# Performance work log

Measured on AMD Instinct MI355X. Metric: run time of the kernel, lower is better.

## Reference

```python
import jax, jax.numpy as jnp
import numpy as np

D = 384      # d_model
DM = 256     # memory feature dim
DF = 1536    # dim_feedforward
EPS = 1e-5


def _layer_norm(x, g, b):
    m = jnp.mean(x, axis=-1, keepdims=True)
    v = jnp.mean(jnp.square(x - m), axis=-1, keepdims=True)
    return (x - m) * jax.lax.rsqrt(v + EPS) * g + b


def setup_inputs() -> dict:
    key = jax.random.key(0)
    ks = jax.random.split(key, 24)
    B, T, T1, Tc = 8, 2048, 2048, 2048
    s = 0.02
    inp = {
        "tgt": jax.random.normal(ks[0], (B, T, D), jnp.float32),
        "memory": jax.random.normal(ks[1], (B, T1, DM), jnp.float32),
        "a1": jnp.float32(0.5),
        "score_c": jax.random.normal(ks[2], (B, 1, Tc, T1), jnp.float32) * 0.1,
        "out_c": jax.random.normal(ks[3], (B, Tc, D), jnp.float32),
        # attention projections
        "Wq": jax.random.normal(ks[4], (D, D), jnp.float32) * s,
        "bq": jnp.zeros((D,), jnp.float32),
        "Wk": jax.random.normal(ks[5], (DM, D), jnp.float32) * s,
        "bk": jnp.zeros((D,), jnp.float32),
        "Wv": jax.random.normal(ks[6], (DM, D), jnp.float32) * s,
        "bv": jnp.zeros((D,), jnp.float32),
        "Wu": jax.random.normal(ks[7], (D, D), jnp.float32) * s,  # unknown
        "bu": jnp.zeros((D,), jnp.float32),
        "Wn": jax.random.normal(ks[8], (D, D), jnp.float32) * s,  # known
        "bn": jnp.zeros((D,), jnp.float32),
        # FFN
        "W1": jax.random.normal(ks[9], (D, DF), jnp.float32) * s,
        "b1": jnp.zeros((DF,), jnp.float32),
        "W2": jax.random.normal(ks[10], (DF, D), jnp.float32) * s,
        "b2": jnp.zeros((D,), jnp.float32),
        # LayerNorms
        "g1": jnp.ones((D,), jnp.float32),
        "be1": jnp.zeros((D,), jnp.float32),
        "g2": jnp.ones((D,), jnp.float32),
        "be2": jnp.zeros((D,), jnp.float32),
    }
    return inp


def reference(tgt, memory, a1, score_c, out_c,
              Wq, bq, Wk, bk, Wv, bv, Wu, bu, Wn, bn,
              W1, b1, W2, b2, g1, be1, g2, be2):
    # --- En_De_Attention (n_head = 1; dropout p=0 / eval mode -> identity) ---
    scale = 1.0 / jnp.sqrt(jnp.float32(D))
    q = tgt @ Wq + bq                  # [B,T,D]
    k = memory @ Wk + bk               # [B,T1,D]
    v = memory @ Wv + bv               # [B,T1,D]
    att = jnp.einsum('btd,bsd->bts', q, k) * scale            # [B,T,T1]

    unknow = tgt @ Wu + bu             # [B,T,D]
    know = out_c @ Wn + bn             # [B,Tc,D]
    score1 = jnp.einsum('btd,bcd->btc', unknow, know) * scale  # [B,T,Tc]
    mixed = jnp.einsum('btc,bcs->bts', score1, score_c[:, 0])  # [B,T,T1]

    # tt = a1 in (0,1]: blended-score branch of the original module
    score = a1 * jax.nn.softmax(mixed, axis=-1) \
          + (1.0 - a1) * jax.nn.softmax(att, axis=-1)          # [B,T,T1]
    z = jnp.einsum('bts,bsd->btd', score, v)                   # [B,T,D]

    # --- residual + norm1 ---
    x = _layer_norm(tgt + z, g1, be1)
    # --- FFN (relu) + residual + norm2 (dropout eval -> identity) ---
    ff = jax.nn.relu(x @ W1 + b1) @ W2 + b2
    out = _layer_norm(x + ff, g2, be2)
    # score2 returned with head dim, matching torch shape [B,1,T,T1]
    return out, score[:, None]
```

## Files before the change

kernel.cpp:

```cpp
#include <hip/hip_runtime.h>
#include <stdint.h>

typedef __attribute__((ext_vector_type(8))) short bf16x8;
typedef __attribute__((ext_vector_type(4))) float f32x4;

__device__ __forceinline__ short f2bf(float f) {
    union { float f; unsigned u; } v; v.f = f;
    unsigned r = v.u + 0x7fffu + ((v.u >> 16) & 1u);
    return (short)(r >> 16);
}
__device__ __forceinline__ float bf2f(short s) {
    union { unsigned u; float f; } v;
    v.u = ((unsigned)(unsigned short)s) << 16;
    return v.f;
}

__device__ __forceinline__ void gld16(const void* g, void* l) {
    auto gp = reinterpret_cast<const __attribute__((address_space(1))) unsigned int*>(
        reinterpret_cast<uintptr_t>(g));
    auto lp = reinterpret_cast<__attribute__((address_space(3))) unsigned int*>(
        reinterpret_cast<uintptr_t>(l));
    __builtin_amdgcn_global_load_lds(gp, lp, 16, 0, 0);
}

template<int OUTBF, int BIASMODE , int DORELU>
__global__ __launch_bounds__(256, 2) void gemm128p(
    const short* __restrict__ Ag, const short* __restrict__ Bg,
    void* __restrict__ Cg, const float* __restrict__ bias,
    int K, int lda, int ldb, int ldc,
    long long sA, long long sB, long long sC, float scale)
{
    __shared__ short lds[2 * 16384];
    const int t = threadIdx.x;
    const int lane = t & 63;
    const int wave = t >> 6;
    const int wm = wave >> 1, wn = wave & 1;

    const int gx = gridDim.x, gy = gridDim.y;
    const int nwg = gx * gy * gridDim.z;
    int id = blockIdx.x + gx * (blockIdx.y + gy * blockIdx.z);
    id = (id & 7) * (nwg >> 3) + (id >> 3);
    const int bx = id % gx;
    const int by = (id / gx) % gy;
    const int bz = id / (gx * gy);

    const long long row0 = (long long)by * 128;
    const long long col0 = (long long)bx * 128;
    const int NT = K >> 6;

    const int srow = t >> 3;
    const int gk = ((t & 7) ^ (srow & 7)) * 8;
    const short* Asrc = Ag + (long long)bz * sA + (row0 + srow) * (long long)lda + gk;
    const short* Bsrc = Bg + (long long)bz * sB + (col0 + srow) * (long long)ldb + gk;

    const int frow = lane & 15;
    const int fq = lane >> 4;

    f32x4 acc[4][4] = {};

#define STAGE_A(WB, KC) do { _Pragma("unroll") \
        for (int r = 0; r < 4; ++r) \
            gld16(Asrc + (KC) + (long long)r * 32 * lda, &lds[(WB) + t * 8 + r * 2048]); } while (0)
#define STAGE_B(WB, KC) do { _Pragma("unroll") \
        for (int r = 0; r < 4; ++r) \
            gld16(Bsrc + (KC) + (long long)r * 32 * ldb, &lds[(WB) + 8192 + t * 8 + r * 2048]); } while (0)
#define RD_A(RB, M, KS) (*(const bf16x8*)&lds[(RB) + (wm * 64 + (M) * 16 + frow) * 64 + \
        ((((KS) << 2) | fq) ^ (frow & 7)) * 8])
#define RD_B(RB, Nn, KS) (*(const bf16x8*)&lds[(RB) + 8192 + (wn * 64 + (Nn) * 16 + frow) * 64 + \
        ((((KS) << 2) | fq) ^ (frow & 7)) * 8])

    STAGE_A(0, 0);
    STAGE_B(0, 0);
    asm volatile("s_waitcnt vmcnt(0)\ns_barrier" ::: "memory");

    for (int kt = 0; kt < NT; ++kt) {
        const int rb = (kt & 1) << 14;
        const int wb = ((kt + 1) & 1) << 14;
        const bool st = (kt + 1) < NT;
        const long long kc = (long long)(kt + 1) << 6;

        bf16x8 av[4], bv[4];

#pragma unroll
        for (int m = 0; m < 4; ++m) av[m] = RD_A(rb, m, 0);
#pragma unroll
        for (int n = 0; n < 4; ++n) bv[n] = RD_B(rb, n, 0);
        if (st) STAGE_A(wb, kc);
        asm volatile("s_barrier" ::: "memory");
        __builtin_amdgcn_s_setprio(1);
#pragma unroll
        for (int m = 0; m < 4; ++m)
#pragma unroll
            for (int n = 0; n < 4; ++n)
                acc[m][n] = __builtin_amdgcn_mfma_f32_16x16x32_bf16(av[m], bv[n], acc[m][n], 0, 0, 0);
        __builtin_amdgcn_s_setprio(0);
        asm volatile("s_barrier" ::: "memory");

#pragma unroll
        for (int m = 0; m < 4; ++m) av[m] = RD_A(rb, m, 1);
#pragma unroll
        for (int n = 0; n < 4; ++n) bv[n] = RD_B(rb, n, 1);
        if (st) STAGE_B(wb, kc);
        asm volatile("s_barrier" ::: "memory");
        __builtin_amdgcn_s_setprio(1);
#pragma unroll
        for (int m = 0; m < 4; ++m)
#pragma unroll
            for (int n = 0; n < 4; ++n)
                acc[m][n] = __builtin_amdgcn_mfma_f32_16x16x32_bf16(av[m], bv[n], acc[m][n], 0, 0, 0);
        __builtin_amdgcn_s_setprio(0);
        if (st) asm volatile("s_waitcnt vmcnt(0)\ns_barrier" ::: "memory");
        else    asm volatile("s_barrier" ::: "memory");
    }
#undef STAGE_A
#undef STAGE_B

    const int crow = (lane >> 4) * 4;
    const int ccol = lane & 15;
    const long long cz = (long long)bz * sC;
#pragma unroll
    for (int m = 0; m < 4; ++m)
#pragma unroll
        for (int n = 0; n < 4; ++n)
#pragma unroll
            for (int i = 0; i < 4; ++i) {
                long long r = row0 + wm * 64 + m * 16 + crow + i;
                long long c = col0 + wn * 64 + n * 16 + ccol;
                float v = acc[m][n][i] * scale;
                if (BIASMODE == 1) v += bias[c];
                if (BIASMODE == 2) v += bias[r];
                if (DORELU) v = fmaxf(v, 0.0f);
                long long idx = cz + r * (long long)ldc + c;
                if (OUTBF) ((short*)Cg)[idx] = f2bf(v);
                else ((float*)Cg)[idx] = v;
            }
}

__global__ __launch_bounds__(256, 2) void gemm128pz(
    const short* __restrict__ A1, const short* __restrict__ B1, short* __restrict__ C1,
    const float* __restrict__ bias1, int K1, int lda1, int ldb1, int ldc1,
    long long sB1, long long sC1,
    const short* __restrict__ A2, const short* __restrict__ B2, short* __restrict__ C2,
    const float* __restrict__ bias2, int K2, int lda2, int ldb2, int ldc2,
    long long sB2, long long sC2)
{
    __shared__ short lds[2 * 16384];
    const int t = threadIdx.x;
    const int lane = t & 63;
    const int wave = t >> 6;
    const int wm = wave >> 1, wn = wave & 1;

    const int gx = gridDim.x, gy = gridDim.y;
    const int nwg = gx * gy * gridDim.z;
    int id = blockIdx.x + gx * (blockIdx.y + gy * blockIdx.z);
    id = (id & 7) * (nwg >> 3) + (id >> 3);
    const int bx = id % gx;
    const int by = (id / gx) % gy;
    const int bz = id / (gx * gy);

    const bool sel = bz >= 8;
    const int zz = bz & 7;
    const short* Ag = sel ? A2 : A1;
    const short* Bg = sel ? B2 : B1;
    short* Cg = sel ? C2 : C1;
    const float* bias = sel ? bias2 : bias1;
    const int K = sel ? K2 : K1;
    const int lda = sel ? lda2 : lda1;
    const int ldb = sel ? ldb2 : ldb1;
    const int ldc = sel ? ldc2 : ldc1;
    const long long sB = sel ? sB2 : sB1;
    const long long sC = sel ? sC2 : sC1;

    const long long row0 = (long long)by * 128;
    const long long col0 = (long long)bx * 128;
    const int NT = K >> 6;

    const int srow = t >> 3;
    const int gk = ((t & 7) ^ (srow & 7)) * 8;
    const short* Asrc = Ag + (row0 + srow) * (long long)lda + gk;
    const short* Bsrc = Bg + (long long)zz * sB + (col0 + srow) * (long long)ldb + gk;

    const int frow = lane & 15;
    const int fq = lane >> 4;

    f32x4 acc[4][4] = {};

#define STAGE_A(WB, KC) do { _Pragma("unroll") \
        for (int r = 0; r < 4; ++r) \
            gld16(Asrc + (KC) + (long long)r * 32 * lda, &lds[(WB) + t * 8 + r * 2048]); } while (0)
#define STAGE_B(WB, KC) do { _Pragma("unroll") \
        for (int r = 0; r < 4; ++r) \
            gld16(Bsrc + (KC) + (long long)r * 32 * ldb, &lds[(WB) + 8192 + t * 8 + r * 2048]); } while (0)

    STAGE_A(0, 0);
    STAGE_B(0, 0);
    asm volatile("s_waitcnt vmcnt(0)\ns_barrier" ::: "memory");

    for (int kt = 0; kt < NT; ++kt) {
        const int rb = (kt & 1) << 14;
        const int wb = ((kt + 1) & 1) << 14;
        const bool st = (kt + 1) < NT;
        const long long kc = (long long)(kt + 1) << 6;

        bf16x8 av[4], bv[4];

#pragma unroll
        for (int m = 0; m < 4; ++m) av[m] = RD_A(rb, m, 0);
#pragma unroll
        for (int n = 0; n < 4; ++n) bv[n] = RD_B(rb, n, 0);
        if (st) STAGE_A(wb, kc);
        asm volatile("s_barrier" ::: "memory");
        __builtin_amdgcn_s_setprio(1);
#pragma unroll
        for (int m = 0; m < 4; ++m)
#pragma unroll
            for (int n = 0; n < 4; ++n)
                acc[m][n] = __builtin_amdgcn_mfma_f32_16x16x32_bf16(av[m], bv[n], acc[m][n], 0, 0, 0);
        __builtin_amdgcn_s_setprio(0);
        asm volatile("s_barrier" ::: "memory");

#pragma unroll
        for (int m = 0; m < 4; ++m) av[m] = RD_A(rb, m, 1);
#pragma unroll
        for (int n = 0; n < 4; ++n) bv[n] = RD_B(rb, n, 1);
        if (st) STAGE_B(wb, kc);
        asm volatile("s_barrier" ::: "memory");
        __builtin_amdgcn_s_setprio(1);
#pragma unroll
        for (int m = 0; m < 4; ++m)
#pragma unroll
            for (int n = 0; n < 4; ++n)
                acc[m][n] = __builtin_amdgcn_mfma_f32_16x16x32_bf16(av[m], bv[n], acc[m][n], 0, 0, 0);
        __builtin_amdgcn_s_setprio(0);
        if (st) asm volatile("s_waitcnt vmcnt(0)\ns_barrier" ::: "memory");
        else    asm volatile("s_barrier" ::: "memory");
    }
#undef STAGE_A
#undef STAGE_B

    const int crow = (lane >> 4) * 4;
    const int ccol = lane & 15;
    const long long cz = (long long)zz * sC;
#pragma unroll
    for (int m = 0; m < 4; ++m)
#pragma unroll
        for (int n = 0; n < 4; ++n)
#pragma unroll
            for (int i = 0; i < 4; ++i) {
                long long r = row0 + wm * 64 + m * 16 + crow + i;
                long long c = col0 + wn * 64 + n * 16 + ccol;
                float v = acc[m][n][i] + bias[r];
                Cg[cz + r * (long long)ldc + c] = f2bf(v);
            }
}

__global__ __launch_bounds__(256, 2) void gemm128dd(
    const short* __restrict__ Ag, const short* __restrict__ Bg, short* __restrict__ Cg,
    int K, int lda, int ldb, int ldc,
    long long sA, long long sB, long long sC,
    int dA, long long dB, long long dC, float scale)
{
    __shared__ short lds[2 * 16384];
    const int t = threadIdx.x;
    const int lane = t & 63;
    const int wave = t >> 6;
    const int wm = wave >> 1, wn = wave & 1;

    const int gx = gridDim.x, gy = gridDim.y;
    const int nwg = gx * gy * gridDim.z;
    int id = blockIdx.x + gx * (blockIdx.y + gy * blockIdx.z);
    id = (id & 7) * (nwg >> 3) + (id >> 3);
    const int bx = id % gx;
    const int by = (id / gx) % gy;
    const int bz = id / (gx * gy);

    const long long row0 = (long long)by * 128;
    const long long col0 = (long long)bx * 128;
    const int NT = K >> 6;

    const int srow = t >> 3;
    const int gk = ((t & 7) ^ (srow & 7)) * 8;
    const short* Asrc = Ag + (long long)bz * sA + (row0 + srow) * (long long)lda + gk;
    const short* Bsrc = Bg + (long long)bz * sB + (col0 + srow) * (long long)ldb + gk;

    const int frow = lane & 15;
    const int fq = lane >> 4;

    f32x4 accA[4][4] = {};
    f32x4 accB[4][4] = {};

#define AOFF(KT2) (((KT2) >= NT) ? ((long long)dA + (long long)((KT2) - NT) * 64) : ((long long)(KT2) * 64))
#define BOFF(KT2) (((KT2) >= NT) ? (dB + (long long)((KT2) - NT) * 64) : ((long long)(KT2) * 64))
#define STAGE_A(WB, OFF) do { _Pragma("unroll") \
        for (int r = 0; r < 4; ++r) \
            gld16(Asrc + (OFF) + (long long)r * 32 * lda, &lds[(WB) + t * 8 + r * 2048]); } while (0)
#define STAGE_B(WB, OFF) do { _Pragma("unroll") \
        for (int r = 0; r < 4; ++r) \
            gld16(Bsrc + (OFF) + (long long)r * 32 * ldb, &lds[(WB) + 8192 + t * 8 + r * 2048]); } while (0)

    STAGE_A(0, 0);
    STAGE_B(0, 0);
    asm volatile("s_waitcnt vmcnt(0)\ns_barrier" ::: "memory");

    const int NT2 = NT * 2;
    for (int kt = 0; kt < NT2; ++kt) {
        const int rb = (kt & 1) << 14;
        const int wb = ((kt + 1) & 1) << 14;
        const bool st = (kt + 1) < NT2;
        const long long ao = AOFF(kt + 1);
        const long long bo = BOFF(kt + 1);
        const bool first = kt < NT;

        bf16x8 av[4], bv[4];

#pragma unroll
        for (int m = 0; m < 4; ++m) av[m] = RD_A(rb, m, 0);
#pragma unroll
        for (int n = 0; n < 4; ++n) bv[n] = RD_B(rb, n, 0);
        if (st) STAGE_A(wb, ao);
        asm volatile("s_barrier" ::: "memory");
        __builtin_amdgcn_s_setprio(1);
        if (first) {
#pragma unroll
            for (int m = 0; m < 4; ++m)
#pragma unroll
                for (int n = 0; n < 4; ++n)
                    accA[m][n] = __builtin_amdgcn_mfma_f32_16x16x32_bf16(av[m], bv[n], accA[m][n], 0, 0, 0);
        } else {
#pragma unroll
            for (int m = 0; m < 4; ++m)
#pragma unroll
                for (int n = 0; n < 4; ++n)
                    accB[m][n] = __builtin_amdgcn_mfma_f32_16x16x32_bf16(av[m], bv[n], accB[m][n], 0, 0, 0);
        }
        __builtin_amdgcn_s_setprio(0);
        asm volatile("s_barrier" ::: "memory");

#pragma unroll
        for (int m = 0; m < 4; ++m) av[m] = RD_A(rb, m, 1);
#pragma unroll
        for (int n = 0; n < 4; ++n) bv[n] = RD_B(rb, n, 1);
        if (st) STAGE_B(wb, bo);
        asm volatile("s_barrier" ::: "memory");
        __builtin_amdgcn_s_setprio(1);
        if (first) {
#pragma unroll
            for (int m = 0; m < 4; ++m)
#pragma unroll
                for (int n = 0; n < 4; ++n)
                    accA[m][n] = __builtin_amdgcn_mfma_f32_16x16x32_bf16(av[m], bv[n], accA[m][n], 0, 0, 0);
        } else {
#pragma unroll
            for (int m = 0; m < 4; ++m)
#pragma unroll
                for (int n = 0; n < 4; ++n)
                    accB[m][n] = __builtin_amdgcn_mfma_f32_16x16x32_bf16(av[m], bv[n], accB[m][n], 0, 0, 0);
        }
        __builtin_amdgcn_s_setprio(0);
        if (st) asm volatile("s_waitcnt vmcnt(0)\ns_barrier" ::: "memory");
        else    asm volatile("s_barrier" ::: "memory");
    }
#undef STAGE_A
#undef STAGE_B
#undef AOFF
#undef BOFF
#undef RD_A
#undef RD_B

    const int crow = (lane >> 4) * 4;
    const int ccol = lane & 15;
    const long long cz = (long long)bz * sC;
#pragma unroll
    for (int m = 0; m < 4; ++m)
#pragma unroll
        for (int n = 0; n < 4; ++n)
#pragma unroll
            for (int i = 0; i < 4; ++i) {
                long long r = row0 + wm * 64 + m * 16 + crow + i;
                long long c = col0 + wn * 64 + n * 16 + ccol;
                long long idx = cz + r * (long long)ldc + c;
                Cg[idx] = f2bf(accA[m][n][i] * scale);
                Cg[idx + dC] = f2bf(accB[m][n][i] * scale);
            }
}

__global__ __launch_bounds__(256) void cast_all(
    const float* __restrict__ tgt, const float* __restrict__ mem, const float* __restrict__ outc,
    const float* __restrict__ bq, const float* __restrict__ bu,
    short* __restrict__ tgtb, short* __restrict__ memb, short* __restrict__ outcb,
    float* __restrict__ qubias)
{
    const long long R1 = 1572864;
    const long long R2 = R1 + 1048576;
    const long long R3 = R2 + 1572864;
    const long long R4 = R3 + 192;
    long long i = (long long)blockIdx.x * 256 + threadIdx.x;
    const float* in; short* out; long long j;
    if (i < R1) { in = tgt; out = tgtb; j = i; }
    else if (i < R2) { in = mem; out = memb; j = i - R1; }
    else if (i < R3) { in = outc; out = outcb; j = i - R2; }
    else if (i < R4) {
        j = i - R3;
        ((float4*)qubias)[j] = (j < 96) ? ((const float4*)bq)[j] : ((const float4*)bu)[j - 96];
        return;
    } else return;
    float4 v = ((const float4*)in)[j];
    short4 o;
    o.x = f2bf(v.x); o.y = f2bf(v.y); o.z = f2bf(v.z); o.w = f2bf(v.w);
    ((short4*)out)[j] = o;
}

__global__ __launch_bounds__(256) void transpose_all(
    const float* __restrict__ Wq, const float* __restrict__ Wk, const float* __restrict__ Wv,
    const float* __restrict__ Wu, const float* __restrict__ Wn,
    const float* __restrict__ W1, const float* __restrict__ W2,
    short* __restrict__ WquT, short* __restrict__ WkT, short* __restrict__ WvT,
    short* __restrict__ WnT, short* __restrict__ W1T, short* __restrict__ W2T)
{
    __shared__ float tile[64][65];
    int b = blockIdx.x;
    const float* in; short* out; int R, C, local;
    if (b < 36)       { in = Wq; out = WquT;          R = 384;  C = 384;  local = b; }
    else if (b < 60)  { in = Wk; out = WkT;           R = 256;  C = 384;  local = b - 36; }
    else if (b < 84)  { in = Wv; out = WvT;           R = 256;  C = 384;  local = b - 60; }
    else if (b < 120) { in = Wu; out = WquT + 147456; R = 384;  C = 384;  local = b - 84; }
    else if (b < 156) { in = Wn; out = WnT;           R = 384;  C = 384;  local = b - 120; }
    else if (b < 300) { in = W1; out = W1T;           R = 384;  C = 1536; local = b - 156; }
    else              { in = W2; out = W2T;           R = 1536; C = 384;  local = b - 300; }
    const int nbx = C >> 6;
    const int r0 = (local / nbx) * 64, c0 = (local % nbx) * 64;
    const int lr = threadIdx.x >> 6, lc = threadIdx.x & 63;
#pragma unroll
    for (int i = 0; i < 16; ++i) {
        int r = lr * 16 + i;
        tile[r][lc] = in[(long long)(r0 + r) * C + c0 + lc];
    }
    __syncthreads();
#pragma unroll
    for (int i = 0; i < 16; ++i) {
        int r = lr * 16 + i;
        out[(long long)(c0 + r) * R + r0 + lc] = f2bf(tile[lc][r]);
    }
}

__global__ __launch_bounds__(256) void transpose_cast(
    const float* __restrict__ in, short* __restrict__ out,
    int R, int C, long long sIn, long long sOut)
{
    __shared__ float tile[64][65];
    const long long zi = (long long)blockIdx.z * sIn;
    const long long zo = (long long)blockIdx.z * sOut;
    const int r0 = blockIdx.y * 64, c0 = blockIdx.x * 64;
    const int lr = threadIdx.x >> 6, lc = threadIdx.x & 63;
#pragma unroll
    for (int i = 0; i < 16; ++i) {
        int r = lr * 16 + i;
        tile[r][lc] = in[zi + (long long)(r0 + r) * C + c0 + lc];
    }
    __syncthreads();
#pragma unroll
    for (int i = 0; i < 16; ++i) {
        int r = lr * 16 + i;
        out[zo + (long long)(c0 + r) * R + r0 + lc] = f2bf(tile[lc][r]);
    }
}

__global__ __launch_bounds__(256) void softmax_blend(
    const short* __restrict__ attb, const short* __restrict__ mixb,
    const float* __restrict__ a1p,
    float* __restrict__ outF, short* __restrict__ outB)
{
    const int S = 2048;
    const long long row = blockIdx.x;
    const short* ar = attb + row * S;
    const short* mr = mixb + row * S;
    const int t = threadIdx.x;
    const int wave = t >> 6;

    bf16x8 a8 = *(const bf16x8*)&ar[t * 8];
    bf16x8 m8 = *(const bf16x8*)&mr[t * 8];
    float av[8], mv[8];
#pragma unroll
    for (int i = 0; i < 8; ++i) { av[i] = bf2f(a8[i]); mv[i] = bf2f(m8[i]); }

    float amax = av[0], mmax = mv[0];
#pragma unroll
    for (int i = 1; i < 8; ++i) { amax = fmaxf(amax, av[i]); mmax = fmaxf(mmax, mv[i]); }
#pragma unroll
    for (int o = 32; o; o >>= 1) {
        amax = fmaxf(amax, __shfl_xor(amax, o));
        mmax = fmaxf(mmax, __shfl_xor(mmax, o));
    }
    __shared__ float red[2][4];
    if ((t & 63) == 0) { red[0][wave] = amax; red[1][wave] = mmax; }
    __syncthreads();
    amax = fmaxf(fmaxf(red[0][0], red[0][1]), fmaxf(red[0][2], red[0][3]));
    mmax = fmaxf(fmaxf(red[1][0], red[1][1]), fmaxf(red[1][2], red[1][3]));

    float asum = 0.f, msum = 0.f;
#pragma unroll
    for (int i = 0; i < 8; ++i) {
        av[i] = __expf(av[i] - amax); asum += av[i];
        mv[i] = __expf(mv[i] - mmax); msum += mv[i];
    }
#pragma unroll
    for (int o = 32; o; o >>= 1) {
        asum += __shfl_xor(asum, o);
        msum += __shfl_xor(msum, o);
    }
    __shared__ float red2[2][4];
    if ((t & 63) == 0) { red2[0][wave] = asum; red2[1][wave] = msum; }
    __syncthreads();
    asum = red2[0][0] + red2[0][1] + red2[0][2] + red2[0][3];
    msum = red2[1][0] + red2[1][1] + red2[1][2] + red2[1][3];

    const float a1 = a1p[0];
    const float wm = a1 / msum;
    const float wa = (1.0f - a1) / asum;

    float o0[8];
    bf16x8 ob;
#pragma unroll
    for (int i = 0; i < 8; ++i) {
        float s = wm * mv[i] + wa * av[i];
        o0[i] = s;
        ob[i] = f2bf(s);
    }
    float4 f0, f1;
    f0.x = o0[0]; f0.y = o0[1]; f0.z = o0[2]; f0.w = o0[3];
    f1.x = o0[4]; f1.y = o0[5]; f1.z = o0[6]; f1.w = o0[7];
    *(float4*)&outF[row * S + t * 8] = f0;
    *(float4*)&outF[row * S + t * 8 + 4] = f1;
    *(bf16x8*)&outB[row * S + t * 8] = ob;
}

template<int WRITE_BF>
__global__ __launch_bounds__(256) void ln_kernel(
    const float* __restrict__ X, const float* __restrict__ Yr,
    const float* __restrict__ g, const float* __restrict__ be,
    float* __restrict__ outF, short* __restrict__ outB)
{
    const int Dm = 384;
    const int wave = threadIdx.x >> 6, lane = threadIdx.x & 63;
    const long long row = (long long)blockIdx.x * 4 + wave;
    const float* x = X + row * Dm;
    const float* y = Yr + row * Dm;
    float h[6];
    float s = 0.f, s2 = 0.f;
#pragma unroll
    for (int j = 0; j < 6; ++j) {
        int c = j * 64 + lane;
        h[j] = x[c] + y[c];
        s += h[j]; s2 += h[j] * h[j];
    }
#pragma unroll
    for (int o = 32; o; o >>= 1) { s += __shfl_xor(s, o); s2 += __shfl_xor(s2, o); }
    const float mean = s * (1.0f / 384.0f);
    const float var = s2 * (1.0f / 384.0f) - mean * mean;
    const float rstd = rsqrtf(var + 1e-5f);
#pragma unroll
    for (int j = 0; j < 6; ++j) {
        int c = j * 64 + lane;
        float v = (h[j] - mean) * rstd * g[c] + be[c];
        outF[row * Dm + c] = v;
        if (WRITE_BF) outB[row * Dm + c] = f2bf(v);
    }
}

extern "C" void kernel_launch(void* const* d_in, const int* in_sizes, int n_in,
                              void* d_out, int out_size, void* d_ws, size_t ws_size,
                              hipStream_t stream) {
    const float* tgt     = (const float*)d_in[0];
    const float* memory  = (const float*)d_in[1];
    const float* a1      = (const float*)d_in[2];
    const float* score_c = (const float*)d_in[3];
    const float* out_c   = (const float*)d_in[4];
    const float* Wq = (const float*)d_in[5];  const float* bq = (const float*)d_in[6];
    const float* Wk = (const float*)d_in[7];  const float* bk = (const float*)d_in[8];
    const float* Wv = (const float*)d_in[9];  const float* bv = (const float*)d_in[10];
    const float* Wu = (const float*)d_in[11]; const float* bu = (const float*)d_in[12];
    const float* Wn = (const float*)d_in[13]; const float* bn = (const float*)d_in[14];
    const float* W1 = (const float*)d_in[15]; const float* b1 = (const float*)d_in[16];
    const float* W2 = (const float*)d_in[17]; const float* b2 = (const float*)d_in[18];
    const float* g1 = (const float*)d_in[19]; const float* be1 = (const float*)d_in[20];
    const float* g2 = (const float*)d_in[21]; const float* be2 = (const float*)d_in[22];

    const long long BT = 16384;
    const long long S2 = 2048LL * 2048;
    const long long PB = 2048LL * 384;
    char* ws = (char*)d_ws;
    size_t off = 0;
    auto A_ = [&](size_t b) { size_t r = off; off += (b + 255) & ~(size_t)255; return r; };

    const size_t oTgtB  = A_(BT * 384 * 2);
    const size_t oMemB  = A_(BT * 256 * 2);
    const size_t oOutcB = A_(BT * 384 * 2);
    const size_t oWquT  = A_(768 * 384 * 2);
    const size_t oWnT   = A_(384 * 384 * 2);
    const size_t oWkT   = A_(384 * 256 * 2);
    const size_t oWvT   = A_(384 * 256 * 2);
    const size_t oW1T   = A_(1536 * 384 * 2);
    const size_t oW2T   = A_(384 * 1536 * 2);
    const size_t oQUb   = A_(768 * 4);
    const size_t oQU    = A_(16 * PB * 2);
    const size_t oKP    = A_(16 * PB * 2);
    const size_t oVT    = A_(8LL * 384 * 2048 * 2);
    const size_t oJ     = A_(8 * S2 * 2);
    const size_t oKr    = A_(8 * S2 * 2);
    const size_t oAM    = A_(16 * S2 * 2);
    const size_t oX     = A_(BT * 384 * 4);
    const size_t oXB    = A_(BT * 384 * 2);

    short* tgt_bf  = (short*)(ws + oTgtB);
    short* mem_bf  = (short*)(ws + oMemB);
    short* outc_bf = (short*)(ws + oOutcB);
    short* WquT = (short*)(ws + oWquT);
    short* WnT  = (short*)(ws + oWnT);
    short* WkT  = (short*)(ws + oWkT);
    short* WvT  = (short*)(ws + oWvT);
    short* W1T  = (short*)(ws + oW1T);
    short* W2T  = (short*)(ws + oW2T);
    float* qu_bias = (float*)(ws + oQUb);
    short* qu_bf  = (short*)(ws + oQU);
    short* k_bf   = (short*)(ws + oKP);
    short* Pt_bf  = k_bf + 8 * PB;
    short* vT_bf  = (short*)(ws + oVT);
    short* score_bf = (short*)(ws + oJ);
    short* scoreCt  = (short*)(ws + oKr);
    float* z_f      = (float*)(ws + oKr);
    short* knoT_bf  = (short*)(ws + oAM);
    short* att_bf   = (short*)(ws + oAM);
    short* mix_bf   = att_bf + 8 * S2;
    short* h_bf     = (short*)(ws + oAM);
    float* ff_f     = (float*)(ws + oAM + 8 * S2 * 2);
    float* x_f  = (float*)(ws + oX);
    short* x_bf = (short*)(ws + oXB);

    float* outMain = (float*)d_out;
    float* outScore = (float*)d_out + 6291456;

    const float SC = 0.05103103630798288f;
    dim3 blk(256);

    cast_all<<<16385, blk, 0, stream>>>(tgt, memory, out_c, bq, bu,
                                        tgt_bf, mem_bf, outc_bf, qu_bias);
    transpose_all<<<444, blk, 0, stream>>>(Wq, Wk, Wv, Wu, Wn, W1, W2,
                                           WquT, WkT, WvT, WnT, W1T, W2T);
    transpose_cast<<<dim3(32, 32, 8), blk, 0, stream>>>(score_c, scoreCt, 2048, 2048, S2, S2);

    gemm128p<1, 1, 0><<<dim3(6, 128, 1), blk, 0, stream>>>(
        tgt_bf, WquT, qu_bf, qu_bias, 384, 384, 384, 768, 0, 0, 0, 1.0f);
    gemm128p<1, 1, 0><<<dim3(3, 128, 1), blk, 0, stream>>>(
        mem_bf, WkT, k_bf, bk, 256, 256, 256, 384, 0, 0, 0, 1.0f);
    gemm128pz<<<dim3(16, 3, 16), blk, 0, stream>>>(
        WvT, mem_bf, vT_bf, bv, 256, 256, 256, 2048, 2048LL * 256, PB,
        WnT, outc_bf, knoT_bf, bn, 384, 384, 384, 2048, PB, PB);
    gemm128p<1, 0, 0><<<dim3(3, 16, 8), blk, 0, stream>>>(
        scoreCt, knoT_bf, Pt_bf, nullptr, 2048, 2048, 2048, 384, S2, PB, PB, 1.0f);
    gemm128dd<<<dim3(16, 16, 8), blk, 0, stream>>>(
        qu_bf, k_bf, att_bf, 384, 768, 384, 2048,
        2048LL * 768, PB, S2, 384, 8 * PB, 8 * S2, SC);
    softmax_blend<<<16384, blk, 0, stream>>>(att_bf, mix_bf, a1, outScore, score_bf);
    gemm128p<0, 0, 0><<<dim3(3, 16, 8), blk, 0, stream>>>(
        score_bf, vT_bf, z_f, nullptr, 2048, 2048, 2048, 384, S2, PB, PB, 1.0f);
    ln_kernel<1><<<4096, blk, 0, stream>>>(tgt, z_f, g1, be1, x_f, x_bf);
    gemm128p<1, 1, 1><<<dim3(12, 128, 1), blk, 0, stream>>>(
        x_bf, W1T, h_bf, b1, 384, 384, 384, 1536, 0, 0, 0, 1.0f);
    gemm128p<0, 1, 0><<<dim3(3, 128, 1), blk, 0, stream>>>(
        h_bf, W2T, ff_f, b2, 1536, 1536, 1536, 384, 0, 0, 0, 1.0f);
    ln_kernel<0><<<4096, blk, 0, stream>>>(x_f, ff_f, g2, be2, outMain, nullptr);
}
```

Before: 460.4 us.

## Replace GEMM with triple-buffered K=32 pipeline and split dual-score GEMM across grid

The double-buffered 64-wide-K GEMM is replaced by a triple-buffered kernel using 32-wide K tiles with a two-stage prefetch, one barrier per iteration, and a new XOR swizzle. LDS use drops, so occupancy rises to 3 blocks per CU. The fused dual-accumulator attention-score GEMM is removed, and its two products now run as separate z-slices of the generic kernel through a grid z of 16 with zlo/zhi strides. The cost is more loop iterations, each with less MFMA work per barrier.

```diff
diff --git a/kernel.cpp b/kernel.cpp
--- a/kernel.cpp
+++ b/kernel.cpp
@@ -24,13 +24,14 @@
 }
 
 template<int OUTBF, int BIASMODE , int DORELU>
-__global__ __launch_bounds__(256, 2) void gemm128p(
+__global__ __launch_bounds__(256, 3) void gemm128r(
     const short* __restrict__ Ag, const short* __restrict__ Bg,
     void* __restrict__ Cg, const float* __restrict__ bias,
     int K, int lda, int ldb, int ldc,
-    long long sA, long long sB, long long sC, float scale)
-{
-    __shared__ short lds[2 * 16384];
+    long long sA, long long sB, long long sC,
+    long long dA, long long dB, long long dC, float scale)
+{
+    __shared__ short lds[3 * 8192];
     const int t = threadIdx.x;
     const int lane = t & 63;
     const int wave = t >> 6;
@@ -43,50 +44,41 @@
     const int bx = id % gx;
     const int by = (id / gx) % gy;
     const int bz = id / (gx * gy);
+    const int zlo = bz & 7, zhi = bz >> 3;
 
     const long long row0 = (long long)by * 128;
     const long long col0 = (long long)bx * 128;
-    const int NT = K >> 6;
-
-    const int srow = t >> 3;
-    const int gk = ((t & 7) ^ (srow & 7)) * 8;
-    const short* Asrc = Ag + (long long)bz * sA + (row0 + srow) * (long long)lda + gk;
-    const short* Bsrc = Bg + (long long)bz * sB + (col0 + srow) * (long long)ldb + gk;
+    const int NT = K >> 5;
+
+    const int gk = ((t & 3) ^ ((t >> 2) & 3) ^ ((t >> 4) & 3)) * 8;
+    const short* Asrc = Ag + zlo * sA + zhi * dA + (row0 + (t >> 2)) * (long long)lda + gk;
+    const short* Bsrc = Bg + zlo * sB + zhi * dB + (col0 + (t >> 2)) * (long long)ldb + gk;
 
     const int frow = lane & 15;
-    const int fq = lane >> 4;
+    const int fcol = ((lane >> 4) ^ (frow & 3) ^ ((frow >> 2) & 3)) * 8;
 
     f32x4 acc[4][4] = {};
 
-#define STAGE_A(WB, KC) do { _Pragma("unroll") \
-        for (int r = 0; r < 4; ++r) \
-            gld16(Asrc + (KC) + (long long)r * 32 * lda, &lds[(WB) + t * 8 + r * 2048]); } while (0)
-#define STAGE_B(WB, KC) do { _Pragma("unroll") \
-        for (int r = 0; r < 4; ++r) \
-            gld16(Bsrc + (KC) + (long long)r * 32 * ldb, &lds[(WB) + 8192 + t * 8 + r * 2048]); } while (0)
-#define RD_A(RB, M, KS) (*(const bf16x8*)&lds[(RB) + (wm * 64 + (M) * 16 + frow) * 64 + \
-        ((((KS) << 2) | fq) ^ (frow & 7)) * 8])
-#define RD_B(RB, Nn, KS) (*(const bf16x8*)&lds[(RB) + 8192 + (wn * 64 + (Nn) * 16 + frow) * 64 + \
-        ((((KS) << 2) | fq) ^ (frow & 7)) * 8])
-
-    STAGE_A(0, 0);
-    STAGE_B(0, 0);
-    asm volatile("s_waitcnt vmcnt(0)\ns_barrier" ::: "memory");
+#define STG(BUF, KC) do { \
+        gld16(Asrc + (KC), &lds[(BUF) * 8192 + t * 8]); \
+        gld16(Asrc + (KC) + 64LL * lda, &lds[(BUF) * 8192 + 2048 + t * 8]); \
+        gld16(Bsrc + (KC), &lds[(BUF) * 8192 + 4096 + t * 8]); \
+        gld16(Bsrc + (KC) + 64LL * ldb, &lds[(BUF) * 8192 + 6144 + t * 8]); } while (0)
+
+    STG(0, 0);
+    STG(1, 32);
+    asm volatile("s_waitcnt vmcnt(4)\ns_barrier" ::: "memory");
 
     for (int kt = 0; kt < NT; ++kt) {
-        const int rb = (kt & 1) << 14;
-        const int wb = ((kt + 1) & 1) << 14;
-        const bool st = (kt + 1) < NT;
-        const long long kc = (long long)(kt + 1) << 6;
-
+        const int rb = (kt % 3) * 8192;
         bf16x8 av[4], bv[4];
-
-#pragma unroll
-        for (int m = 0; m < 4; ++m) av[m] = RD_A(rb, m, 0);
-#pragma unroll
-        for (int n = 0; n < 4; ++n) bv[n] = RD_B(rb, n, 0);
-        if (st) STAGE_A(wb, kc);
-        asm volatile("s_barrier" ::: "memory");
+#pragma unroll
+        for (int m = 0; m < 4; ++m)
+            av[m] = *(const bf16x8*)&lds[rb + (wm * 64 + m * 16 + frow) * 32 + fcol];
+#pragma unroll
+        for (int n = 0; n < 4; ++n)
+            bv[n] = *(const bf16x8*)&lds[rb + 4096 + (wn * 64 + n * 16 + frow) * 32 + fcol];
+        if (kt + 2 < NT) STG((kt + 2) % 3, (long long)(kt + 2) * 32);
         __builtin_amdgcn_s_setprio(1);
 #pragma unroll
         for (int m = 0; m < 4; ++m)
@@ -94,30 +86,16 @@
             for (int n = 0; n < 4; ++n)
                 acc[m][n] = __builtin_amdgcn_mfma_f32_16x16x32_bf16(av[m], bv[n], acc[m][n], 0, 0, 0);
         __builtin_amdgcn_s_setprio(0);
-        asm volatile("s_barrier" ::: "memory");
-
-#pragma unroll
-        for (int m = 0; m < 4; ++m) av[m] = RD_A(rb, m, 1);
-#pragma unroll
-        for (int n = 0; n < 4; ++n) bv[n] = RD_B(rb, n, 1);
-        if (st) STAGE_B(wb, kc);
-        asm volatile("s_barrier" ::: "memory");
-        __builtin_amdgcn_s_setprio(1);
-#pragma unroll
-        for (int m = 0; m < 4; ++m)
-#pragma unroll
-            for (int n = 0; n < 4; ++n)
-                acc[m][n] = __builtin_amdgcn_mfma_f32_16x16x32_bf16(av[m], bv[n], acc[m][n], 0, 0, 0);
-        __builtin_amdgcn_s_setprio(0);
-        if (st) asm volatile("s_waitcnt vmcnt(0)\ns_barrier" ::: "memory");
-        else    asm volatile("s_barrier" ::: "memory");
-    }
-#undef STAGE_A
-#undef STAGE_B
+        if (kt + 1 < NT) {
+            if (kt + 2 < NT) asm volatile("s_waitcnt vmcnt(4)\ns_barrier" ::: "memory");
+            else             asm volatile("s_waitcnt vmcnt(0)\ns_barrier" ::: "memory");
+        }
+    }
+#undef STG
 
     const int crow = (lane >> 4) * 4;
     const int ccol = lane & 15;
-    const long long cz = (long long)bz * sC;
+    const long long cz = zlo * sC + zhi * dC;
 #pragma unroll
     for (int m = 0; m < 4; ++m)
 #pragma unroll
@@ -135,6 +113,11 @@
                 else ((float*)Cg)[idx] = v;
             }
 }
+
+#define RD_A(RB, M, KS) (*(const bf16x8*)&lds[(RB) + (wm * 64 + (M) * 16 + frow) * 64 + \
+        ((((KS) << 2) | fq) ^ (frow & 7)) * 8])
+#define RD_B(RB, Nn, KS) (*(const bf16x8*)&lds[(RB) + 8192 + (wn * 64 + (Nn) * 16 + frow) * 64 + \
+        ((((KS) << 2) | fq) ^ (frow & 7)) * 8])
 
 __global__ __launch_bounds__(256, 2) void gemm128pz(
     const short* __restrict__ A1, const short* __restrict__ B1, short* __restrict__ C1,
@@ -253,136 +236,8 @@
                 Cg[cz + r * (long long)ldc + c] = f2bf(v);
             }
 }
-
-__global__ __launch_bounds__(256, 2) void gemm128dd(
-    const short* __restrict__ Ag, const short* __restrict__ Bg, short* __restrict__ Cg,
-    int K, int lda, int ldb, int ldc,
-    long long sA, long long sB, long long sC,
-    int dA, long long dB, long long dC, float scale)
-{
-    __shared__ short lds[2 * 16384];
-    const int t = threadIdx.x;
-    const int lane = t & 63;
-    const int wave = t >> 6;
-    const int wm = wave >> 1, wn = wave & 1;
-
-    const int gx = gridDim.x, gy = gridDim.y;
-    const int nwg = gx * gy * gridDim.z;
-    int id = blockIdx.x + gx * (blockIdx.y + gy * blockIdx.z);
-    id = (id & 7) * (nwg >> 3) + (id >> 3);
-    const int bx = id % gx;
-    const int by = (id / gx) % gy;
-    const int bz = id / (gx * gy);
-
-    const long long row0 = (long long)by * 128;
-    const long long col0 = (long long)bx * 128;
-    const int NT = K >> 6;
-
-    const int srow = t >> 3;
-    const int gk = ((t & 7) ^ (srow & 7)) * 8;
-    const short* Asrc = Ag + (long long)bz * sA + (row0 + srow) * (long long)lda + gk;
-    const short* Bsrc = Bg + (long long)bz * sB + (col0 + srow) * (long long)ldb + gk;
-
-    const int frow = lane & 15;
-    const int fq = lane >> 4;
-
-    f32x4 accA[4][4] = {};
-    f32x4 accB[4][4] = {};
-
-#define AOFF(KT2) (((KT2) >= NT) ? ((long long)dA + (long long)((KT2) - NT) * 64) : ((long long)(KT2) * 64))
-#define BOFF(KT2) (((KT2) >= NT) ? (dB + (long long)((KT2) - NT) * 64) : ((long long)(KT2) * 64))
-#define STAGE_A(WB, OFF) do { _Pragma("unroll") \
-        for (int r = 0; r < 4; ++r) \
-            gld16(Asrc + (OFF) + (long long)r * 32 * lda, &lds[(WB) + t * 8 + r * 2048]); } while (0)
-#define STAGE_B(WB, OFF) do { _Pragma("unroll") \
-        for (int r = 0; r < 4; ++r) \
-            gld16(Bsrc + (OFF) + (long long)r * 32 * ldb, &lds[(WB) + 8192 + t * 8 + r * 2048]); } while (0)
-
-    STAGE_A(0, 0);
-    STAGE_B(0, 0);
-    asm volatile("s_waitcnt vmcnt(0)\ns_barrier" ::: "memory");
-
-    const int NT2 = NT * 2;
-    for (int kt = 0; kt < NT2; ++kt) {
-        const int rb = (kt & 1) << 14;
-        const int wb = ((kt + 1) & 1) << 14;
-        const bool st = (kt + 1) < NT2;
-        const long long ao = AOFF(kt + 1);
-        const long long bo = BOFF(kt + 1);
-        const bool first = kt < NT;
-
-        bf16x8 av[4], bv[4];
-
-#pragma unroll
-        for (int m = 0; m < 4; ++m) av[m] = RD_A(rb, m, 0);
-#pragma unroll
-        for (int n = 0; n < 4; ++n) bv[n] = RD_B(rb, n, 0);
-        if (st) STAGE_A(wb, ao);
-        asm volatile("s_barrier" ::: "memory");
-        __builtin_amdgcn_s_setprio(1);
-        if (first) {
-#pragma unroll
-            for (int m = 0; m < 4; ++m)
-#pragma unroll
-                for (int n = 0; n < 4; ++n)
-                    accA[m][n] = __builtin_amdgcn_mfma_f32_16x16x32_bf16(av[m], bv[n], accA[m][n], 0, 0, 0);
-        } else {
-#pragma unroll
-            for (int m = 0; m < 4; ++m)
-#pragma unroll
-                for (int n = 0; n < 4; ++n)
-                    accB[m][n] = __builtin_amdgcn_mfma_f32_16x16x32_bf16(av[m], bv[n], accB[m][n], 0, 0, 0);
-        }
-        __builtin_amdgcn_s_setprio(0);
-        asm volatile("s_barrier" ::: "memory");
-
-#pragma unroll
-        for (int m = 0; m < 4; ++m) av[m] = RD_A(rb, m, 1);
-#pragma unroll
-        for (int n = 0; n < 4; ++n) bv[n] = RD_B(rb, n, 1);
-        if (st) STAGE_B(wb, bo);
-        asm volatile("s_barrier" ::: "memory");
-        __builtin_amdgcn_s_setprio(1);
-        if (first) {
-#pragma unroll
-            for (int m = 0; m < 4; ++m)
-#pragma unroll
-                for (int n = 0; n < 4; ++n)
-                    accA[m][n] = __builtin_amdgcn_mfma_f32_16x16x32_bf16(av[m], bv[n], accA[m][n], 0, 0, 0);
-        } else {
-#pragma unroll
-            for (int m = 0; m < 4; ++m)
-#pragma unroll
-                for (int n = 0; n < 4; ++n)
-                    accB[m][n] = __builtin_amdgcn_mfma_f32_16x16x32_bf16(av[m], bv[n], accB[m][n], 0, 0, 0);
-        }
-        __builtin_amdgcn_s_setprio(0);
-        if (st) asm volatile("s_waitcnt vmcnt(0)\ns_barrier" ::: "memory");
-        else    asm volatile("s_barrier" ::: "memory");
-    }
-#undef STAGE_A
-#undef STAGE_B
-#undef AOFF
-#undef BOFF
 #undef RD_A
 #undef RD_B
-
-    const int crow = (lane >> 4) * 4;
-    const int ccol = lane & 15;
-    const long long cz = (long long)bz * sC;
-#pragma unroll
-    for (int m = 0; m < 4; ++m)
-#pragma unroll
-        for (int n = 0; n < 4; ++n)
-#pragma unroll
-            for (int i = 0; i < 4; ++i) {
-                long long r = row0 + wm * 64 + m * 16 + crow + i;
-                long long c = col0 + wn * 64 + n * 16 + ccol;
-                long long idx = cz + r * (long long)ldc + c;
-                Cg[idx] = f2bf(accA[m][n][i] * scale);
-                Cg[idx + dC] = f2bf(accB[m][n][i] * scale);
-            }
-}
 
 __global__ __launch_bounds__(256) void cast_all(
     const float* __restrict__ tgt, const float* __restrict__ mem, const float* __restrict__ outc,
@@ -648,25 +503,27 @@
                                            WquT, WkT, WvT, WnT, W1T, W2T);
     transpose_cast<<<dim3(32, 32, 8), blk, 0, stream>>>(score_c, scoreCt, 2048, 2048, S2, S2);
 
-    gemm128p<1, 1, 0><<<dim3(6, 128, 1), blk, 0, stream>>>(
-        tgt_bf, WquT, qu_bf, qu_bias, 384, 384, 384, 768, 0, 0, 0, 1.0f);
-    gemm128p<1, 1, 0><<<dim3(3, 128, 1), blk, 0, stream>>>(
-        mem_bf, WkT, k_bf, bk, 256, 256, 256, 384, 0, 0, 0, 1.0f);
+    gemm128r<1, 1, 0><<<dim3(6, 128, 1), blk, 0, stream>>>(
+        tgt_bf, WquT, qu_bf, qu_bias, 384, 384, 384, 768, 0, 0, 0, 0, 0, 0, 1.0f);
+    gemm128r<1, 1, 0><<<dim3(3, 128, 1), blk, 0, stream>>>(
+        mem_bf, WkT, k_bf, bk, 256, 256, 256, 384, 0, 0, 0, 0, 0, 0, 1.0f);
     gemm128pz<<<dim3(16, 3, 16), blk, 0, stream>>>(
         WvT, mem_bf, vT_bf, bv, 256, 256, 256, 2048, 2048LL * 256, PB,
         WnT, outc_bf, knoT_bf, bn, 384, 384, 384, 2048, PB, PB);
-    gemm128p<1, 0, 0><<<dim3(3, 16, 8), blk, 0, stream>>>(
-        scoreCt, knoT_bf, Pt_bf, nullptr, 2048, 2048, 2048, 384, S2, PB, PB, 1.0f);
-    gemm128dd<<<dim3(16, 16, 8), blk, 0, stream>>>(
-        qu_bf, k_bf, att_bf, 384, 768, 384, 2048,
+    gemm128r<1, 0, 0><<<dim3(3, 16, 8), blk, 0, stream>>>(
+        scoreCt, knoT_bf, Pt_bf, nullptr, 2048, 2048, 2048, 384,
+        S2, PB, PB, 0, 0, 0, 1.0f);
+    gemm128r<1, 0, 0><<<dim3(16, 16, 16), blk, 0, stream>>>(
+        qu_bf, k_bf, att_bf, nullptr, 384, 768, 384, 2048,
         2048LL * 768, PB, S2, 384, 8 * PB, 8 * S2, SC);
     softmax_blend<<<16384, blk, 0, stream>>>(att_bf, mix_bf, a1, outScore, score_bf);
-    gemm128p<0, 0, 0><<<dim3(3, 16, 8), blk, 0, stream>>>(
-        score_bf, vT_bf, z_f, nullptr, 2048, 2048, 2048, 384, S2, PB, PB, 1.0f);
+    gemm128r<0, 0, 0><<<dim3(3, 16, 8), blk, 0, stream>>>(
+        score_bf, vT_bf, z_f, nullptr, 2048, 2048, 2048, 384,
+        S2, PB, PB, 0, 0, 0, 1.0f);
     ln_kernel<1><<<4096, blk, 0, stream>>>(tgt, z_f, g1, be1, x_f, x_bf);
-    gemm128p<1, 1, 1><<<dim3(12, 128, 1), blk, 0, stream>>>(
-        x_bf, W1T, h_bf, b1, 384, 384, 384, 1536, 0, 0, 0, 1.0f);
-    gemm128p<0, 1, 0><<<dim3(3, 128, 1), blk, 0, stream>>>(
-        h_bf, W2T, ff_f, b2, 1536, 1536, 1536, 384, 0, 0, 0, 1.0f);
+    gemm128r<1, 1, 1><<<dim3(12, 128, 1), blk, 0, stream>>>(
+        x_bf, W1T, h_bf, b1, 384, 384, 384, 1536, 0, 0, 0, 0, 0, 0, 1.0f);
+    gemm128r<0, 1, 0><<<dim3(3, 128, 1), blk, 0, stream>>>(
+        h_bf, W2T, ff_f, b2, 1536, 1536, 1536, 384, 0, 0, 0, 0, 0, 0, 1.0f);
     ln_kernel<0><<<4096, blk, 0, stream>>>(x_f, ff_f, g2, be2, outMain, nullptr);
 }
```

Result: no change. 456.3 us (-0.9%).
